# Performance work log

Hardware: AMD Instinct MI355X
Metric: run time of the kernel (lower is better)

## Reference

```python
import jax, jax.numpy as jnp
import numpy as np
import math

VOCAB = 32000
D = 2048
H = 16
KVH = 4
HD = D // H          # 128
FF = 5632
L = 2
S = 2048
B = 1
EPS = 1e-5
ROPE_BASE = 10000.0


def setup_inputs() -> dict:
    key = jax.random.key(0)
    ks = jax.random.split(key, 12)
    sc = 0.02
    # RoPE table: [S, HD//2, 2] (cos, sin), matching precompute_freqs_cis
    inv = 1.0 / (ROPE_BASE ** (jnp.arange(0, HD, 2, dtype=jnp.float32) / HD))
    pos = jnp.arange(S, dtype=jnp.float32)
    f = jnp.outer(pos, inv)
    freqs_cis = jnp.stack([jnp.cos(f), jnp.sin(f)], axis=-1)
    mask = jnp.tril(jnp.ones((S, S), dtype=bool))
    return {
        "input_ids": jax.random.randint(ks[0], (B, S), 0, VOCAB, dtype=jnp.int32),
        "mask": mask,
        "freqs_cis": freqs_cis,
        "w_embed": jax.random.normal(ks[1], (VOCAB, D), jnp.float32) * sc,
        "wqkv": jax.random.normal(ks[2], (L, D, D + 2 * KVH * HD), jnp.float32) * sc,
        "wo": jax.random.normal(ks[3], (L, D, D), jnp.float32) * sc,
        "w1": jax.random.normal(ks[4], (L, D, FF), jnp.float32) * sc,
        "w3": jax.random.normal(ks[5], (L, D, FF), jnp.float32) * sc,
        "w2": jax.random.normal(ks[6], (L, FF, D), jnp.float32) * sc,
        "attn_norm_w": jnp.ones((L, D), jnp.float32),
        "ff_norm_w": jnp.ones((L, D), jnp.float32),
        "final_norm_w": jnp.ones((D,), jnp.float32),
        "w_head": jax.random.normal(ks[7], (D, VOCAB), jnp.float32) * sc,
    }


def _rmsnorm(x, w):
    xf = x.astype(jnp.float32)
    n = xf * jax.lax.rsqrt(jnp.mean(xf * xf, axis=-1, keepdims=True) + EPS)
    return n.astype(x.dtype) * w


def _rope(x, fc):
    # x: [b, h, s, hd]; fc: [s, hd/2, 2]
    xr = x.reshape(*x.shape[:-1], HD // 2, 2)
    cos, sin = fc[..., 0], fc[..., 1]  # [s, hd/2] broadcast over b,h
    out = jnp.stack([xr[..., 0] * cos - xr[..., 1] * sin,
                     xr[..., 1] * cos + xr[..., 0] * sin], axis=-1)
    return out.reshape(x.shape).astype(x.dtype)


def _attention(x, mask, fc, wqkv, wo):
    b, s, _ = x.shape
    qkv = x @ wqkv  # [b, s, D + 2*kv_dim]
    kv_dim = KVH * HD
    q, k, v = jnp.split(qkv, [D, D + kv_dim], axis=-1)
    q = q.reshape(b, s, H, HD).transpose(0, 2, 1, 3)      # [b,H,s,hd]
    k = k.reshape(b, s, KVH, HD).transpose(0, 2, 1, 3)    # [b,KVH,s,hd]
    v = v.reshape(b, s, KVH, HD).transpose(0, 2, 1, 3)
    q = _rope(q, fc)
    k = _rope(k, fc)
    rep = H // KVH
    k = jnp.repeat(k, rep, axis=1)  # [b,H,s,hd]
    v = jnp.repeat(v, rep, axis=1)
    scores = jnp.einsum('bhqd,bhkd->bhqk', q, k) / math.sqrt(HD)
    scores = jnp.where(mask, scores, -1e30)
    attn = jax.nn.softmax(scores, axis=-1)
    out = jnp.einsum('bhqk,bhkd->bhqd', attn, v)
    out = out.transpose(0, 2, 1, 3).reshape(b, s, D)
    return out @ wo


def reference(input_ids, mask, freqs_cis, w_embed, wqkv, wo, w1, w3, w2,
              attn_norm_w, ff_norm_w, final_norm_w, w_head):
    x = w_embed[input_ids]  # [B,S,D]
    for l in range(L):
        h = x + _attention(_rmsnorm(x, attn_norm_w[l]), mask, freqs_cis,
                           wqkv[l], wo[l])
        hn = _rmsnorm(h, ff_norm_w[l])
        x = h + (jax.nn.silu(hn @ w1[l]) * (hn @ w3[l])) @ w2[l]
    x = _rmsnorm(x, final_norm_w)
    return x @ w_head  # [B,S,VOCAB]
```

## Files before the change

kernel.cpp:

```cpp
#include <hip/hip_runtime.h>

#define DD 2048
#define SEQ 2048
#define NH 16
#define NKV 4
#define HD 128
#define FFD 5632
#define NL 2

typedef __bf16 bf16x8 __attribute__((ext_vector_type(8)));
typedef float f32x4 __attribute__((ext_vector_type(4)));

__device__ __forceinline__ unsigned short f2bf(float f) {
    unsigned int u = __builtin_bit_cast(unsigned int, f);
    u += 0x7fffu + ((u >> 16) & 1u);
    return (unsigned short)(u >> 16);
}

__global__ __launch_bounds__(256)
void embed_gather(const int* __restrict__ ids, const float* __restrict__ wemb,
                  float* __restrict__ x)
{
    int s = blockIdx.x;
    int id = ids[s];
    const float4* src = (const float4*)(wemb + (size_t)id * DD);
    float4* dst = (float4*)(x + (size_t)s * DD);
    dst[threadIdx.x] = src[threadIdx.x];
    dst[threadIdx.x + 256] = src[threadIdx.x + 256];
}

__global__ __launch_bounds__(256)
void rmsnorm_bf16(const float* __restrict__ x, const float* __restrict__ w,
                  unsigned short* __restrict__ out)
{
    int row = blockIdx.x;
    int t = threadIdx.x;
    const float4* xr = (const float4*)(x + (size_t)row * DD);
    float4 v0 = xr[t], v1 = xr[t + 256];
    float ss = v0.x * v0.x + v0.y * v0.y + v0.z * v0.z + v0.w * v0.w
             + v1.x * v1.x + v1.y * v1.y + v1.z * v1.z + v1.w * v1.w;
#pragma unroll
    for (int off = 32; off; off >>= 1) ss += __shfl_down(ss, off);
    __shared__ float red[4];
    if ((t & 63) == 0) red[t >> 6] = ss;
    __syncthreads();
    float sc = rsqrtf((red[0] + red[1] + red[2] + red[3]) * (1.0f / DD) + 1e-5f);
    const float4* wr = (const float4*)w;
    float4 w0 = wr[t], w1v = wr[t + 256];
    ushort4 o0, o1;
    o0.x = f2bf(v0.x * sc * w0.x);  o0.y = f2bf(v0.y * sc * w0.y);
    o0.z = f2bf(v0.z * sc * w0.z);  o0.w = f2bf(v0.w * sc * w0.w);
    o1.x = f2bf(v1.x * sc * w1v.x); o1.y = f2bf(v1.y * sc * w1v.y);
    o1.z = f2bf(v1.z * sc * w1v.z); o1.w = f2bf(v1.w * sc * w1v.w);
    ushort4* op = (ushort4*)(out + (size_t)row * DD);
    op[t] = o0;
    op[t + 256] = o1;
}

__global__ __launch_bounds__(256)
void transpose_cast(const float* __restrict__ src, unsigned short* __restrict__ dst,
                    int ld_src, int ld_dst, size_t sb, size_t db)
{
    __shared__ float tile[64][65];
    src += (size_t)blockIdx.z * sb;
    dst += (size_t)blockIdx.z * db;
    int c0 = blockIdx.x * 64, r0 = blockIdx.y * 64;
    int tx = threadIdx.x & 15, ty = threadIdx.x >> 4;
#pragma unroll
    for (int i = 0; i < 4; ++i) {
        int r = ty + i * 16;
        float4 v = *(const float4*)(src + (size_t)(r0 + r) * ld_src + c0 + tx * 4);
        tile[r][tx * 4 + 0] = v.x; tile[r][tx * 4 + 1] = v.y;
        tile[r][tx * 4 + 2] = v.z; tile[r][tx * 4 + 3] = v.w;
    }
    __syncthreads();
#pragma unroll
    for (int i = 0; i < 4; ++i) {
        int c = ty + i * 16;
        ushort4 o;
        o.x = f2bf(tile[tx * 4 + 0][c]); o.y = f2bf(tile[tx * 4 + 1][c]);
        o.z = f2bf(tile[tx * 4 + 2][c]); o.w = f2bf(tile[tx * 4 + 3][c]);
        *(ushort4*)(dst + (size_t)(c0 + c) * ld_dst + r0 + tx * 4) = o;
    }
}

__global__ void rope_qk(const float* __restrict__ qkv, const float* __restrict__ fc,
                        unsigned short* __restrict__ Qb, unsigned short* __restrict__ Kb)
{
    int s = blockIdx.x;
    int hh = blockIdx.y;
    int i = threadIdx.x;
    float2 cs = *(const float2*)(fc + ((size_t)s * 64 + i) * 2);
    const float* src;
    unsigned short* dst;
    if (hh < NH) {
        src = qkv + (size_t)s * 3072 + hh * HD;
        dst = Qb + ((size_t)hh * SEQ + s) * HD;
    } else {
        int kh = hh - NH;
        src = qkv + (size_t)s * 3072 + DD + kh * HD;
        dst = Kb + ((size_t)kh * SEQ + s) * HD;
    }
    float2 xv = *(const float2*)(src + 2 * i);
    ushort2 o;
    o.x = f2bf(xv.x * cs.x - xv.y * cs.y);
    o.y = f2bf(xv.y * cs.x + xv.x * cs.y);
    *(ushort2*)(dst + 2 * i) = o;
}

__global__ __launch_bounds__(256)
void silu_mul(const float* __restrict__ h, unsigned short* __restrict__ g)
{
    size_t i = (size_t)blockIdx.x * 256 + threadIdx.x;
    size_t row = i / (FFD / 4), c4 = i % (FFD / 4);
    const float* p = h + row * (2 * FFD) + c4 * 4;
    float4 a = *(const float4*)(p);
    float4 b = *(const float4*)(p + FFD);
    ushort4 o;
    o.x = f2bf(a.x / (1.f + __expf(-a.x)) * b.x);
    o.y = f2bf(a.y / (1.f + __expf(-a.y)) * b.y);
    o.z = f2bf(a.z / (1.f + __expf(-a.z)) * b.z);
    o.w = f2bf(a.w / (1.f + __expf(-a.w)) * b.w);
    *(ushort4*)(g + row * FFD + c4 * 4) = o;
}

__global__ __launch_bounds__(256)
void gemm_bf16(const unsigned short* __restrict__ A, const unsigned short* __restrict__ B,
               float* __restrict__ C, const float* __restrict__ Res,
               int N, int K, int mT)
{
    __shared__ __attribute__((aligned(16))) unsigned char smem[65536];
    const int tid = threadIdx.x;
    const int lane = tid & 63;
    const int w = tid >> 6;
    const int nwg = gridDim.x;
    const int qq = nwg >> 3;
    const int logical = ((int)blockIdx.x & 7) * qq + ((int)blockIdx.x >> 3);
    const int m0 = (logical % mT) * 128;
    const int n0 = (logical / mT) * 128;
    const int wm = (w >> 1) * 64, wn = (w & 1) * 64;
    const int lrow = lane & 15, lgrp = lane >> 4;
    const int NT = K >> 6;

    f32x4 acc[4][4];
#pragma unroll
    for (int i = 0; i < 4; ++i)
#pragma unroll
        for (int j = 0; j < 4; ++j) acc[i][j] = 0.f;

    auto stage = [&](int bsel, int kt) {
#pragma unroll
        for (int it = 0; it < 4; ++it) {
            int o = it * 4096 + tid * 16;
            int row = o >> 7;
            int col = (o & 127) ^ ((row & 7) << 4);
            const char* ga = (const char*)A + ((size_t)(m0 + row) * K + kt) * 2 + col;
            const char* gb = (const char*)B + ((size_t)(n0 + row) * K + kt) * 2 + col;
            __builtin_amdgcn_global_load_lds(
                (__attribute__((address_space(1))) const void*)ga,
                (__attribute__((address_space(3))) void*)(smem + bsel * 32768 + it * 4096 + w * 1024),
                16, 0, 0);
            __builtin_amdgcn_global_load_lds(
                (__attribute__((address_space(1))) const void*)gb,
                (__attribute__((address_space(3))) void*)(smem + bsel * 32768 + 16384 + it * 4096 + w * 1024),
                16, 0, 0);
        }
    };

    stage(0, 0);
    int cur = 0;
    for (int t = 0; t < NT; ++t) {
        if (t + 1 < NT) {
            stage(cur ^ 1, (t + 1) << 6);
            asm volatile("s_waitcnt vmcnt(8)" ::: "memory");
        } else {
            asm volatile("s_waitcnt vmcnt(0)" ::: "memory");
        }
        __builtin_amdgcn_s_barrier();
        __builtin_amdgcn_sched_barrier(0);
        const unsigned char* buf = smem + cur * 32768;
#pragma unroll
        for (int kk = 0; kk < 2; ++kk) {
            bf16x8 af[4], bfr[4];
            int cb = kk * 64 + lgrp * 16;
#pragma unroll
            for (int i = 0; i < 4; ++i) {
                int ra = wm + i * 16 + lrow;
                af[i] = *(const bf16x8*)(buf + ra * 128 + (cb ^ ((ra & 7) << 4)));
                int rb = wn + i * 16 + lrow;
                bfr[i] = *(const bf16x8*)(buf + 16384 + rb * 128 + (cb ^ ((rb & 7) << 4)));
            }
#pragma unroll
            for (int i = 0; i < 4; ++i)
#pragma unroll
                for (int j = 0; j < 4; ++j)
                    acc[i][j] = __builtin_amdgcn_mfma_f32_16x16x32_bf16(af[i], bfr[j], acc[i][j], 0, 0, 0);
        }
        __builtin_amdgcn_s_barrier();
        cur ^= 1;
    }

    const bool hasRes = (Res != nullptr);
#pragma unroll
    for (int i = 0; i < 4; ++i)
#pragma unroll
        for (int j = 0; j < 4; ++j) {
            int r = m0 + wm + i * 16 + lgrp * 4;
            int c = n0 + wn + j * 16 + lrow;
#pragma unroll
            for (int jj = 0; jj < 4; ++jj) {
                size_t idx = (size_t)(r + jj) * N + c;
                float v = acc[i][j][jj];
                if (hasRes) v += Res[idx];
                C[idx] = v;
            }
        }
}

__global__ __launch_bounds__(512, 1)
void gemm_bf16_256(const unsigned short* __restrict__ A, const unsigned short* __restrict__ B,
                   float* __restrict__ C, int N, int K, int mT)
{
    __shared__ __attribute__((aligned(16))) unsigned char smem[131072];
    const int tid = threadIdx.x;
    const int lane = tid & 63;
    const int w = tid >> 6;
    const int nwg = gridDim.x;
    const int qq = nwg >> 3;
    const int logical = ((int)blockIdx.x & 7) * qq + ((int)blockIdx.x >> 3);
    const int m0 = (logical % mT) * 256;
    const int n0 = (logical / mT) * 256;
    const int wm2 = (w >> 2) * 128;
    const int wn4 = (w & 3) * 64;
    const int lrow = lane & 15, lgrp = lane >> 4;
    const int NT = K >> 6;

    f32x4 acc[8][4];
#pragma unroll
    for (int i = 0; i < 8; ++i)
#pragma unroll
        for (int j = 0; j < 4; ++j) acc[i][j] = 0.f;

    auto stage = [&](int bsel, int kt, int pair) {
        int o = pair * 8192 + tid * 16;
        int row = o >> 7;
        int col = (o & 127) ^ ((row & 7) << 4);
        const char* ga = (const char*)A + ((size_t)(m0 + row) * K + kt) * 2 + col;
        const char* gb = (const char*)B + ((size_t)(n0 + row) * K + kt) * 2 + col;
        __builtin_amdgcn_global_load_lds(
            (__attribute__((address_space(1))) const void*)ga,
            (__attribute__((address_space(3))) void*)(smem + bsel * 65536 + pair * 8192 + w * 1024),
            16, 0, 0);
        __builtin_amdgcn_global_load_lds(
            (__attribute__((address_space(1))) const void*)gb,
            (__attribute__((address_space(3))) void*)(smem + bsel * 65536 + 32768 + pair * 8192 + w * 1024),
            16, 0, 0);
    };

#pragma unroll
    for (int p = 0; p < 4; ++p) stage(0, 0, p);

    int cur = 0;
    for (int t = 0; t < NT; ++t) {
        const bool havenext = (t + 1 < NT);
        const int ktn = (t + 1) << 6;
        const unsigned char* buf = smem + cur * 65536;
        bf16x8 bfr[4][2];
#pragma unroll
        for (int p = 0; p < 4; ++p) {
            if (p == 0) {
                if (havenext) {
                    stage(cur ^ 1, ktn, 0);
                    asm volatile("s_waitcnt vmcnt(2)" ::: "memory");
                } else {
                    asm volatile("s_waitcnt vmcnt(0)" ::: "memory");
                }
                __builtin_amdgcn_s_barrier();
                __builtin_amdgcn_sched_barrier(0);
#pragma unroll
                for (int nj = 0; nj < 4; ++nj)
#pragma unroll
                    for (int kk = 0; kk < 2; ++kk) {
                        int rb = wn4 + nj * 16 + lrow;
                        int cb = kk * 64 + lgrp * 16;
                        bfr[nj][kk] = *(const bf16x8*)(buf + 32768 + rb * 128 + (cb ^ ((rb & 7) << 4)));
                    }
            } else {
                if (havenext) stage(cur ^ 1, ktn, p);
                __builtin_amdgcn_s_barrier();
            }
            bf16x8 afr[2][2];
#pragma unroll
            for (int i = 0; i < 2; ++i)
#pragma unroll
                for (int kk = 0; kk < 2; ++kk) {
                    int ra = wm2 + (p * 2 + i) * 16 + lrow;
                    int cb = kk * 64 + lgrp * 16;
                    afr[i][kk] = *(const bf16x8*)(buf + ra * 128 + (cb ^ ((ra & 7) << 4)));
                }
            __builtin_amdgcn_s_setprio(1);
#pragma unroll
            for (int i = 0; i < 2; ++i)
#pragma unroll
                for (int nj = 0; nj < 4; ++nj)
#pragma unroll
                    for (int kk = 0; kk < 2; ++kk)
                        acc[p * 2 + i][nj] = __builtin_amdgcn_mfma_f32_16x16x32_bf16(
                            afr[i][kk], bfr[nj][kk], acc[p * 2 + i][nj], 0, 0, 0);
            __builtin_amdgcn_s_setprio(0);
        }
        __builtin_amdgcn_s_barrier();
        cur ^= 1;
    }

#pragma unroll
    for (int mi = 0; mi < 8; ++mi)
#pragma unroll
        for (int nj = 0; nj < 4; ++nj) {
            int r = m0 + wm2 + mi * 16 + lgrp * 4;
            int c = n0 + wn4 + nj * 16 + lrow;
#pragma unroll
            for (int jj = 0; jj < 4; ++jj)
                C[(size_t)(r + jj) * N + c] = acc[mi][nj][jj];
        }
}

__global__ __launch_bounds__(256)
void attn_fwd(const unsigned short* __restrict__ Qb, const unsigned short* __restrict__ Kb,
              const unsigned short* __restrict__ VTb, unsigned short* __restrict__ O)
{
    __shared__ __attribute__((aligned(16))) unsigned char smem[40960];
    const int qb = 31 - (int)blockIdx.x;
    const int h = blockIdx.y;
    const int kvh = h >> 2;
    const int tid = threadIdx.x, lane = tid & 63, w = tid >> 6;
    const int lrow = lane & 15, lgrp = lane >> 4;
    const int q0 = qb * 64 + w * 16;

    bf16x8 qf[4];
    const unsigned short* qrow = Qb + ((size_t)h * SEQ + q0 + lrow) * HD;
#pragma unroll
    for (int c = 0; c < 4; ++c)
        qf[c] = *(const bf16x8*)(qrow + c * 32 + lgrp * 8);

    float m[4], l[4];
    f32x4 oacc[8];
#pragma unroll
    for (int j = 0; j < 8; ++j) oacc[j] = 0.f;
#pragma unroll
    for (int j = 0; j < 4; ++j) { m[j] = -3.0e38f; l[j] = 0.f; }

    const float scale = 0.08838834764831845f;
    const char* kbase = (const char*)(Kb + (size_t)kvh * SEQ * HD);
    const char* vbase = (const char*)(VTb + (size_t)kvh * HD * SEQ);
    unsigned char* Pl = smem + 32768 + w * 2048;

    for (int t = 0; t <= qb; ++t) {
        __syncthreads();
#pragma unroll
        for (int it = 0; it < 4; ++it) {
            int o = it * 4096 + tid * 16;
            int row = o >> 8, col = o & 255;
            bf16x8 kv = *(const bf16x8*)(kbase + (size_t)(t * 64 + row) * 256 + col);
            *(bf16x8*)(smem + (o ^ ((row & 7) << 4))) = kv;
            int row2 = o >> 7, col2 = o & 127;
            bf16x8 vv = *(const bf16x8*)(vbase + (size_t)row2 * (SEQ * 2) + (size_t)t * 128 + col2);
            *(bf16x8*)(smem + 16384 + (o ^ ((row2 & 7) << 4))) = vv;
        }
        __syncthreads();

        f32x4 sf[4];
#pragma unroll
        for (int kf = 0; kf < 4; ++kf) sf[kf] = 0.f;
#pragma unroll
        for (int kf = 0; kf < 4; ++kf) {
            int rb = kf * 16 + lrow;
            int rbase = rb * 256;
            int sw = (rb & 7) << 4;
#pragma unroll
            for (int c = 0; c < 4; ++c) {
                bf16x8 kfr = *(const bf16x8*)(smem + rbase + ((c * 64 + lgrp * 16) ^ sw));
                sf[kf] = __builtin_amdgcn_mfma_f32_16x16x32_bf16(qf[c], kfr, sf[kf], 0, 0, 0);
            }
        }
        const bool diag = (t == qb);
        float mx[4] = {-3.0e38f, -3.0e38f, -3.0e38f, -3.0e38f};
#pragma unroll
        for (int kf = 0; kf < 4; ++kf)
#pragma unroll
            for (int j = 0; j < 4; ++j) {
                float v = sf[kf][j] * scale;
                if (diag && (t * 64 + kf * 16 + lrow) > (q0 + lgrp * 4 + j)) v = -3.0e38f;
                sf[kf][j] = v;
                mx[j] = fmaxf(mx[j], v);
            }
#pragma unroll
        for (int off = 1; off < 16; off <<= 1)
#pragma unroll
            for (int j = 0; j < 4; ++j) mx[j] = fmaxf(mx[j], __shfl_xor(mx[j], off));
        float alpha[4], rs[4];
#pragma unroll
        for (int j = 0; j < 4; ++j) {
            float mn = fmaxf(m[j], mx[j]);
            alpha[j] = __expf(m[j] - mn);
            m[j] = mn;
            rs[j] = 0.f;
        }
#pragma unroll
        for (int kf = 0; kf < 4; ++kf)
#pragma unroll
            for (int j = 0; j < 4; ++j) {
                float p = __expf(sf[kf][j] - m[j]);
                rs[j] += p;
                int qq = lgrp * 4 + j;
                int addr = qq * 128 + (((kf * 16 + lrow) * 2) ^ ((qq & 7) << 4));
                *(unsigned short*)(Pl + addr) = f2bf(p);
            }
#pragma unroll
        for (int off = 1; off < 16; off <<= 1)
#pragma unroll
            for (int j = 0; j < 4; ++j) rs[j] += __shfl_xor(rs[j], off);
#pragma unroll
        for (int j = 0; j < 4; ++j) l[j] = l[j] * alpha[j] + rs[j];
#pragma unroll
        for (int hf = 0; hf < 8; ++hf)
#pragma unroll
            for (int j = 0; j < 4; ++j) oacc[hf][j] *= alpha[j];
#pragma unroll
        for (int c = 0; c < 2; ++c) {
            int cb = c * 64 + lgrp * 16;
            bf16x8 pf = *(const bf16x8*)(Pl + lrow * 128 + (cb ^ ((lrow & 7) << 4)));
#pragma unroll
            for (int hf = 0; hf < 8; ++hf) {
                int rv = hf * 16 + lrow;
                bf16x8 vf = *(const bf16x8*)(smem + 16384 + rv * 128 + (cb ^ ((rv & 7) << 4)));
                oacc[hf] = __builtin_amdgcn_mfma_f32_16x16x32_bf16(pf, vf, oacc[hf], 0, 0, 0);
            }
        }
    }
#pragma unroll
    for (int hf = 0; hf < 8; ++hf)
#pragma unroll
        for (int j = 0; j < 4; ++j) {
            float v = oacc[hf][j] / l[j];
            int qg = q0 + lgrp * 4 + j;
            O[(size_t)qg * DD + h * HD + hf * 16 + lrow] = f2bf(v);
        }
}

extern "C" void kernel_launch(void* const* d_in, const int* in_sizes, int n_in,
                              void* d_out, int out_size, void* d_ws, size_t ws_size,
                              hipStream_t stream)
{
    (void)in_sizes; (void)n_in; (void)out_size; (void)ws_size;
    const int* ids = (const int*)d_in[0];
    const float* fc   = (const float*)d_in[2];
    const float* wemb = (const float*)d_in[3];
    const float* wqkv = (const float*)d_in[4];
    const float* wo   = (const float*)d_in[5];
    const float* w1   = (const float*)d_in[6];
    const float* w3   = (const float*)d_in[7];
    const float* w2   = (const float*)d_in[8];
    const float* anw  = (const float*)d_in[9];
    const float* fnw  = (const float*)d_in[10];
    const float* finw = (const float*)d_in[11];
    const float* wh   = (const float*)d_in[12];
    float* out = (float*)d_out;
    char* ws = (char*)d_ws;

    unsigned short* WQKVT = (unsigned short*)(ws);
    unsigned short* WOT   = (unsigned short*)(ws + 25165824);
    unsigned short* W13T  = (unsigned short*)(ws + 41943040);
    unsigned short* W2T   = (unsigned short*)(ws + 134217728);
    unsigned short* WHT   = (unsigned short*)(ws + 180355072);
    float*          X     = (float*)(ws + 311427072);
    unsigned short* XN    = (unsigned short*)(ws + 328204288);
    float*          QKV   = (float*)(ws + 336592896);
    unsigned short* Qb    = (unsigned short*)(ws + 361758720);
    unsigned short* Kb    = (unsigned short*)(ws + 370147328);
    unsigned short* VT    = (unsigned short*)(ws + 372244480);
    unsigned short* AO    = (unsigned short*)(ws + 374341632);
    float*          H13   = (float*)(ws + 382730240);
    unsigned short* G     = (unsigned short*)(ws + 475004928);

    transpose_cast<<<dim3(48, 32, 2), 256, 0, stream>>>(wqkv, WQKVT, 3072, 2048,
        (size_t)2048 * 3072, (size_t)3072 * 2048);
    transpose_cast<<<dim3(32, 32, 2), 256, 0, stream>>>(wo, WOT, 2048, 2048,
        (size_t)2048 * 2048, (size_t)2048 * 2048);
    transpose_cast<<<dim3(88, 32, 2), 256, 0, stream>>>(w1, W13T, 5632, 2048,
        (size_t)2048 * 5632, (size_t)11264 * 2048);
    transpose_cast<<<dim3(88, 32, 2), 256, 0, stream>>>(w3, W13T + (size_t)5632 * 2048, 5632, 2048,
        (size_t)2048 * 5632, (size_t)11264 * 2048);
    transpose_cast<<<dim3(32, 88, 2), 256, 0, stream>>>(w2, W2T, 2048, 5632,
        (size_t)5632 * 2048, (size_t)2048 * 5632);
    transpose_cast<<<dim3(500, 32, 1), 256, 0, stream>>>(wh, WHT, 32000, 2048, 0, 0);

    embed_gather<<<dim3(SEQ), 256, 0, stream>>>(ids, wemb, X);

    for (int lyr = 0; lyr < NL; ++lyr) {
        const unsigned short* wqkvT_l = WQKVT + (size_t)lyr * 3072 * 2048;
        const unsigned short* woT_l   = WOT   + (size_t)lyr * 2048 * 2048;
        const unsigned short* w13T_l  = W13T  + (size_t)lyr * 11264 * 2048;
        const unsigned short* w2T_l   = W2T   + (size_t)lyr * 2048 * 5632;

        rmsnorm_bf16<<<dim3(SEQ), 256, 0, stream>>>(X, anw + lyr * DD, XN);
        gemm_bf16<<<dim3(24 * 16), 256, 0, stream>>>(XN, wqkvT_l, QKV, nullptr, 3072, 2048, 16);
        rope_qk<<<dim3(SEQ, NH + NKV), 64, 0, stream>>>(QKV, fc, Qb, Kb);
        transpose_cast<<<dim3(2, 32, 4), 256, 0, stream>>>(QKV + 2560, VT, 3072, 2048,
            128, (size_t)128 * 2048);
        attn_fwd<<<dim3(32, NH), 256, 0, stream>>>(Qb, Kb, VT, AO);
        gemm_bf16<<<dim3(16 * 16), 256, 0, stream>>>(AO, woT_l, X, X, 2048, 2048, 16);
        rmsnorm_bf16<<<dim3(SEQ), 256, 0, stream>>>(X, fnw + lyr * DD, XN);
        gemm_bf16_256<<<dim3(8 * 44), 512, 0, stream>>>(XN, w13T_l, H13, 11264, 2048, 8);
        silu_mul<<<dim3(11264), 256, 0, stream>>>(H13, G);
        gemm_bf16<<<dim3(16 * 16), 256, 0, stream>>>(G, w2T_l, X, X, 2048, 5632, 16);
    }
    rmsnorm_bf16<<<dim3(SEQ), 256, 0, stream>>>(X, finw, XN);
    gemm_bf16_256<<<dim3(8 * 125), 512, 0, stream>>>(XN, WHT, out, 32000, 2048, 8);
}
```

Before: 1.315 ms.

## Double-buffer attention K/V via async LDS loads and batch GEMM prefetch issue

The attention kernel now stages K and V tiles with direct global-to-LDS loads into a double buffer and prefetches the next tile while computing the current one. This replaces the synchronous load-then-store-then-syncthreads pattern. The GEMM kernel issues its whole next-tile prefetch at the top of each k-step and drops the per-subtile barriers, leaving one barrier per tile. Attention shared memory rises to 72KB, which may lower occupancy, and the GEMM loses the finer interleaving of loads with MFMA work.

```diff
diff --git a/kernel.cpp b/kernel.cpp
--- a/kernel.cpp
+++ b/kernel.cpp
@@ -241,60 +241,53 @@
 #pragma unroll
         for (int j = 0; j < 4; ++j) acc[i][j] = 0.f;
 
-    auto stage = [&](int bsel, int kt, int pair) {
-        int o = pair * 8192 + tid * 16;
-        int row = o >> 7;
-        int col = (o & 127) ^ ((row & 7) << 4);
-        const char* ga = (const char*)A + ((size_t)(m0 + row) * K + kt) * 2 + col;
-        const char* gb = (const char*)B + ((size_t)(n0 + row) * K + kt) * 2 + col;
-        __builtin_amdgcn_global_load_lds(
-            (__attribute__((address_space(1))) const void*)ga,
-            (__attribute__((address_space(3))) void*)(smem + bsel * 65536 + pair * 8192 + w * 1024),
-            16, 0, 0);
-        __builtin_amdgcn_global_load_lds(
-            (__attribute__((address_space(1))) const void*)gb,
-            (__attribute__((address_space(3))) void*)(smem + bsel * 65536 + 32768 + pair * 8192 + w * 1024),
-            16, 0, 0);
+    auto stage_all = [&](int bsel, int kt) {
+#pragma unroll
+        for (int it = 0; it < 8; ++it) {
+            int o = (it & 3) * 8192 + tid * 16;
+            int row = o >> 7;
+            int col = (o & 127) ^ ((row & 7) << 4);
+            const unsigned short* base = (it < 4) ? A : B;
+            int r0 = (it < 4) ? m0 : n0;
+            const char* g = (const char*)base + ((size_t)(r0 + row) * K + kt) * 2 + col;
+            __builtin_amdgcn_global_load_lds(
+                (__attribute__((address_space(1))) const void*)g,
+                (__attribute__((address_space(3))) void*)(smem + bsel * 65536 +
+                    (it < 4 ? 0 : 32768) + (it & 3) * 8192 + w * 1024),
+                16, 0, 0);
+        }
     };
 
-#pragma unroll
-    for (int p = 0; p < 4; ++p) stage(0, 0, p);
-
+    stage_all(0, 0);
     int cur = 0;
     for (int t = 0; t < NT; ++t) {
-        const bool havenext = (t + 1 < NT);
-        const int ktn = (t + 1) << 6;
+        if (t + 1 < NT) {
+            stage_all(cur ^ 1, (t + 1) << 6);
+            asm volatile("s_waitcnt vmcnt(8)" ::: "memory");
+        } else {
+            asm volatile("s_waitcnt vmcnt(0)" ::: "memory");
+        }
+        __builtin_amdgcn_s_barrier();
+        __builtin_amdgcn_sched_barrier(0);
         const unsigned char* buf = smem + cur * 65536;
+
         bf16x8 bfr[4][2];
 #pragma unroll
-        for (int p = 0; p < 4; ++p) {
-            if (p == 0) {
-                if (havenext) {
-                    stage(cur ^ 1, ktn, 0);
-                    asm volatile("s_waitcnt vmcnt(2)" ::: "memory");
-                } else {
-                    asm volatile("s_waitcnt vmcnt(0)" ::: "memory");
-                }
-                __builtin_amdgcn_s_barrier();
-                __builtin_amdgcn_sched_barrier(0);
-#pragma unroll
-                for (int nj = 0; nj < 4; ++nj)
-#pragma unroll
-                    for (int kk = 0; kk < 2; ++kk) {
-                        int rb = wn4 + nj * 16 + lrow;
-                        int cb = kk * 64 + lgrp * 16;
-                        bfr[nj][kk] = *(const bf16x8*)(buf + 32768 + rb * 128 + (cb ^ ((rb & 7) << 4)));
-                    }
-            } else {
-                if (havenext) stage(cur ^ 1, ktn, p);
-                __builtin_amdgcn_s_barrier();
-            }
+        for (int nj = 0; nj < 4; ++nj)
+#pragma unroll
+            for (int kk = 0; kk < 2; ++kk) {
+                int rb = wn4 + nj * 16 + lrow;
+                int cb = kk * 64 + lgrp * 16;
+                bfr[nj][kk] = *(const bf16x8*)(buf + 32768 + rb * 128 + (cb ^ ((rb & 7) << 4)));
+            }
+#pragma unroll
+        for (int mp = 0; mp < 4; ++mp) {
             bf16x8 afr[2][2];
 #pragma unroll
             for (int i = 0; i < 2; ++i)
 #pragma unroll
                 for (int kk = 0; kk < 2; ++kk) {
-                    int ra = wm2 + (p * 2 + i) * 16 + lrow;
+                    int ra = wm2 + (mp * 2 + i) * 16 + lrow;
                     int cb = kk * 64 + lgrp * 16;
                     afr[i][kk] = *(const bf16x8*)(buf + ra * 128 + (cb ^ ((ra & 7) << 4)));
                 }
@@ -305,8 +298,8 @@
                 for (int nj = 0; nj < 4; ++nj)
 #pragma unroll
                     for (int kk = 0; kk < 2; ++kk)
-                        acc[p * 2 + i][nj] = __builtin_amdgcn_mfma_f32_16x16x32_bf16(
-                            afr[i][kk], bfr[nj][kk], acc[p * 2 + i][nj], 0, 0, 0);
+                        acc[mp * 2 + i][nj] = __builtin_amdgcn_mfma_f32_16x16x32_bf16(
+                            afr[i][kk], bfr[nj][kk], acc[mp * 2 + i][nj], 0, 0, 0);
             __builtin_amdgcn_s_setprio(0);
         }
         __builtin_amdgcn_s_barrier();
@@ -329,7 +322,7 @@
 void attn_fwd(const unsigned short* __restrict__ Qb, const unsigned short* __restrict__ Kb,
               const unsigned short* __restrict__ VTb, unsigned short* __restrict__ O)
 {
-    __shared__ __attribute__((aligned(16))) unsigned char smem[40960];
+    __shared__ __attribute__((aligned(16))) unsigned char smem[73728];
     const int qb = 31 - (int)blockIdx.x;
     const int h = blockIdx.y;
     const int kvh = h >> 2;
@@ -353,21 +346,46 @@
     const float scale = 0.08838834764831845f;
     const char* kbase = (const char*)(Kb + (size_t)kvh * SEQ * HD);
     const char* vbase = (const char*)(VTb + (size_t)kvh * HD * SEQ);
-    unsigned char* Pl = smem + 32768 + w * 2048;
-
-    for (int t = 0; t <= qb; ++t) {
-        __syncthreads();
+    unsigned char* Pl = smem + 65536 + w * 2048;
+
+    auto stage_kv = [&](int bsel, int t) {
 #pragma unroll
         for (int it = 0; it < 4; ++it) {
             int o = it * 4096 + tid * 16;
             int row = o >> 8, col = o & 255;
-            bf16x8 kv = *(const bf16x8*)(kbase + (size_t)(t * 64 + row) * 256 + col);
-            *(bf16x8*)(smem + (o ^ ((row & 7) << 4))) = kv;
-            int row2 = o >> 7, col2 = o & 127;
-            bf16x8 vv = *(const bf16x8*)(vbase + (size_t)row2 * (SEQ * 2) + (size_t)t * 128 + col2);
-            *(bf16x8*)(smem + 16384 + (o ^ ((row2 & 7) << 4))) = vv;
-        }
-        __syncthreads();
+            int scol = col ^ ((row & 7) << 4);
+            const char* g = kbase + (size_t)(t * 64 + row) * 256 + scol;
+            __builtin_amdgcn_global_load_lds(
+                (__attribute__((address_space(1))) const void*)g,
+                (__attribute__((address_space(3))) void*)(smem + bsel * 32768 + it * 4096 + w * 1024),
+                16, 0, 0);
+        }
+#pragma unroll
+        for (int it = 0; it < 4; ++it) {
+            int o = it * 4096 + tid * 16;
+            int row = o >> 7, col = o & 127;
+            int scol = col ^ ((row & 7) << 4);
+            const char* g = vbase + (size_t)row * (SEQ * 2) + (size_t)t * 128 + scol;
+            __builtin_amdgcn_global_load_lds(
+                (__attribute__((address_space(1))) const void*)g,
+                (__attribute__((address_space(3))) void*)(smem + bsel * 32768 + 16384 + it * 4096 + w * 1024),
+                16, 0, 0);
+        }
+    };
+
+    stage_kv(0, 0);
+    int cur = 0;
+    for (int t = 0; t <= qb; ++t) {
+        if (t < qb) {
+            stage_kv(cur ^ 1, t + 1);
+            asm volatile("s_waitcnt vmcnt(8)" ::: "memory");
+        } else {
+            asm volatile("s_waitcnt vmcnt(0)" ::: "memory");
+        }
+        __builtin_amdgcn_s_barrier();
+        __builtin_amdgcn_sched_barrier(0);
+        const unsigned char* kb = smem + cur * 32768;
+        const unsigned char* vtb = kb + 16384;
 
         f32x4 sf[4];
 #pragma unroll
@@ -379,7 +397,7 @@
             int sw = (rb & 7) << 4;
 #pragma unroll
             for (int c = 0; c < 4; ++c) {
-                bf16x8 kfr = *(const bf16x8*)(smem + rbase + ((c * 64 + lgrp * 16) ^ sw));
+                bf16x8 kfr = *(const bf16x8*)(kb + rbase + ((c * 64 + lgrp * 16) ^ sw));
                 sf[kf] = __builtin_amdgcn_mfma_f32_16x16x32_bf16(qf[c], kfr, sf[kf], 0, 0, 0);
             }
         }
@@ -433,10 +451,12 @@
 #pragma unroll
             for (int hf = 0; hf < 8; ++hf) {
                 int rv = hf * 16 + lrow;
-                bf16x8 vf = *(const bf16x8*)(smem + 16384 + rv * 128 + (cb ^ ((rv & 7) << 4)));
+                bf16x8 vf = *(const bf16x8*)(vtb + rv * 128 + (cb ^ ((rv & 7) << 4)));
                 oacc[hf] = __builtin_amdgcn_mfma_f32_16x16x32_bf16(pf, vf, oacc[hf], 0, 0, 0);
             }
         }
+        __builtin_amdgcn_s_barrier();
+        cur ^= 1;
     }
 #pragma unroll
     for (int hf = 0; hf < 8; ++hf)
```

New measurement: 1.283 ms. 1.02x faster.
